# Optimization experiments

Hardware: AMD Instinct MI355X
Metric: run time of the kernel (lower is better)

The kernel has to match this reference:

```python
import jax, jax.numpy as jnp
import numpy as np

B, T, V = 32, 100, 20000
E, H, M, DD = 128, 128, 64, 2


def setup_inputs() -> dict:
    key = jax.random.key(0)
    ks = jax.random.split(key, 12)
    x = jax.random.uniform(ks[0], (B, T, V), dtype=jnp.float32)
    # zero out trailing timesteps per example so Masking layer matters
    lens = jax.random.randint(ks[1], (B,), T * 3 // 4, T + 1)
    tmask = (jnp.arange(T)[None, :] < lens[:, None]).astype(jnp.float32)
    x = x * tmask[:, :, None]
    a = jax.random.uniform(ks[2], (B, V), dtype=jnp.float32)
    d = jax.random.normal(ks[3], (B, DD), dtype=jnp.float32)
    # parameters
    emb = jax.random.uniform(ks[4], (V, E), minval=-0.1, maxval=0.1, dtype=jnp.float32)
    s = 1.0 / np.sqrt(E)
    gru_k = jax.random.uniform(ks[5], (E, 3 * H), minval=-s, maxval=s, dtype=jnp.float32)
    gru_rk = jax.random.normal(ks[6], (H, 3 * H), dtype=jnp.float32) / np.sqrt(H)
    gru_b_i = jnp.zeros((3 * H,), jnp.float32)   # input bias (reset_after=True)
    gru_b_r = jnp.zeros((3 * H,), jnp.float32)   # recurrent bias
    s1 = 1.0 / np.sqrt(H + E)
    W1 = jax.random.uniform(ks[7], (H + E, M), minval=-s1, maxval=s1, dtype=jnp.float32)
    b1 = jnp.zeros((M,), jnp.float32)
    s2 = 1.0 / np.sqrt(M + DD)
    W2 = jax.random.uniform(ks[8], (M + DD, 1), minval=-s2, maxval=s2, dtype=jnp.float32)
    b2 = jnp.zeros((1,), jnp.float32)
    return dict(x=x, a=a, d=d, emb=emb, gru_k=gru_k, gru_rk=gru_rk,
                gru_b_i=gru_b_i, gru_b_r=gru_b_r, W1=W1, b1=b1, W2=W2, b2=b2)


def _gru_final_state(xe, mask, gru_k, gru_rk, gru_b_i, gru_b_r):
    # xe: [B,T,E], mask: [B,T] bool. Keras GRU, reset_after=True, eval mode (dropout off).
    Hn = gru_rk.shape[0]
    x_proj = jnp.einsum('bte,eh->bth', xe, gru_k) + gru_b_i  # [B,T,3H]

    def step(h, inp):
        xp_t, m_t = inp                      # [B,3H], [B]
        rec = h @ gru_rk + gru_b_r           # [B,3H]
        xz, xr, xh = jnp.split(xp_t, 3, axis=-1)
        rz, rr, rh = jnp.split(rec, 3, axis=-1)
        z = jax.nn.sigmoid(xz + rz)
        r = jax.nn.sigmoid(xr + rr)
        hh = jnp.tanh(xh + r * rh)
        h_new = z * h + (1.0 - z) * hh
        h = jnp.where(m_t[:, None], h_new, h)  # masked steps carry state
        return h, None

    h0 = jnp.zeros((xe.shape[0], Hn), xe.dtype)
    h_final, _ = jax.lax.scan(step, h0, (jnp.swapaxes(x_proj, 0, 1), jnp.swapaxes(mask, 0, 1)))
    return h_final


def reference(x, a, d, emb, gru_k, gru_rk, gru_b_i, gru_b_r, W1, b1, W2, b2):
    ae = jnp.tanh(a @ emb)                       # [B,E]
    xe = jnp.tanh(jnp.einsum('btv,ve->bte', x, emb))  # [B,T,E]
    mask = jnp.any(xe != 0.0, axis=-1)           # Masking(mask_value=0.0)
    h = _gru_final_state(xe, mask, gru_k, gru_rk, gru_b_i, gru_b_r)  # [B,H]
    c = jnp.tanh(jnp.concatenate([h, ae], axis=1) @ W1 + b1)         # [B,M]
    out = jax.nn.sigmoid(jnp.concatenate([c, d], axis=1) @ W2 + b2)  # [B,1]
    return out
```

## Files before the change

### kernel.cpp

```cpp
#include <hip/hip_runtime.h>

typedef __attribute__((ext_vector_type(8))) short short8;
typedef __attribute__((ext_vector_type(4))) float float4v;

#define V_ 20000

__device__ __forceinline__ unsigned short f2bf(float f) {
    union { float f; unsigned int u; } v; v.f = f;
    unsigned int u = v.u;
    u += 0x7fffu + ((u >> 16) & 1u);
    return (unsigned short)(u >> 16);
}

__device__ __forceinline__ float fast_tanh(float x) {
    float xc = fminf(15.f, fmaxf(-15.f, x));
    float e = __expf(2.f * xc);
    return (e - 1.f) / (e + 1.f);
}

__device__ __forceinline__ float sigmoidf_(float x) {
    float xc = fminf(30.f, fmaxf(-30.f, x));
    return 1.f / (1.f + __expf(-xc));
}

#define GLL16(gp, lp) __builtin_amdgcn_global_load_lds( \
    (const __attribute__((address_space(1))) void*)(gp), \
    (__attribute__((address_space(3))) void*)(lp), 16, 0, 0)

__global__ __launch_bounds__(256) void cvt_embT(const float* __restrict__ emb,
                                                unsigned short* __restrict__ embT,
                                                float* __restrict__ xeacc) {
    int tid = threadIdx.x;
    int gid = blockIdx.x * 256 + tid;
    for (int i = gid; i < 3328 * 128; i += 313 * 256) xeacc[i] = 0.f;

    __shared__ unsigned short tile[128 * 65];
    int k0 = blockIdx.x * 64;
    const float4v* e4 = (const float4v*)emb;
    #pragma unroll
    for (int c = 0; c < 8; ++c) {
        int l4 = c * 256 + tid;
        int k = l4 >> 5;
        int n4 = l4 & 31;
        float4v f = {0.f, 0.f, 0.f, 0.f};
        if (k0 + k < V_) f = e4[(size_t)(k0 + k) * 32 + n4];
        tile[(n4 * 4 + 0) * 65 + k] = f2bf(f.x);
        tile[(n4 * 4 + 1) * 65 + k] = f2bf(f.y);
        tile[(n4 * 4 + 2) * 65 + k] = f2bf(f.z);
        tile[(n4 * 4 + 3) * 65 + k] = f2bf(f.w);
    }
    __syncthreads();
    #pragma unroll
    for (int c = 0; c < 4; ++c) {
        int l8 = c * 256 + tid;
        int n = l8 >> 3, seg = l8 & 7;
        int kk = k0 + seg * 8;
        if (kk < V_) {
            short8 v;
            #pragma unroll
            for (int i = 0; i < 8; ++i) v[i] = (short)tile[n * 65 + seg * 8 + i];
            *(short8*)(embT + (size_t)n * V_ + kk) = v;
        }
    }
}

__global__ __launch_bounds__(256, 4) void big_gemm(const float* __restrict__ x,
                                                   const float* __restrict__ a,
                                                   const unsigned short* __restrict__ embT,
                                                   float* __restrict__ xeacc,
                                                   int ks) {
    __shared__ unsigned short Alds[2][128 * 40];
    __shared__ unsigned short Blds[2][128 * 32];
    int tid = threadIdx.x;
    int bx = blockIdx.x, by = blockIdx.y;
    int m0 = bx * 128;
    int per = 625 / ks, extra = 625 % ks;
    int kb0 = by * per + (by < extra ? by : extra);
    int nkb = per + (by < extra ? 1 : 0);

    int lane = tid & 63, wave = tid >> 6;
    int wr = wave >> 1, wc = wave & 1;
    int ln = lane & 15, quad = lane >> 4;

    float4v acc[4][4];
    #pragma unroll
    for (int i = 0; i < 4; ++i)
        #pragma unroll
        for (int j = 0; j < 4; ++j) acc[i][j] = (float4v){0.f, 0.f, 0.f, 0.f};

    int row = tid >> 1, seg = tid & 1;
    int rg = m0 + row;
    int aidx = rg - 3200; aidx = aidx < 0 ? 0 : (aidx > 31 ? 31 : aidx);
    const float* __restrict__ srcA = (rg < 3200) ? (x + (size_t)rg * V_)
                                                 : (a + (size_t)aidx * V_);
    int brow0 = tid >> 2, bkq = tid & 3;
    int wbase = tid & ~63;
    const unsigned short* gB0 = embT + (size_t)brow0 * V_ + bkq * 8;
    const unsigned short* gB1 = embT + (size_t)(64 + brow0) * V_ + bkq * 8;

    float4v fa0, fa1, fa2, fa3;

    {
        int k0 = kb0 * 32;
        const float4v* ap = (const float4v*)(srcA + k0 + seg * 16);
        fa0 = ap[0]; fa1 = ap[1]; fa2 = ap[2]; fa3 = ap[3];
        GLL16(gB0 + k0, &Blds[0][(size_t)wbase * 8]);
        GLL16(gB1 + k0, &Blds[0][(size_t)(256 + wbase) * 8]);
        short8 w0, w1;
        w0[0]=(short)f2bf(fa0.x); w0[1]=(short)f2bf(fa0.y); w0[2]=(short)f2bf(fa0.z); w0[3]=(short)f2bf(fa0.w);
        w0[4]=(short)f2bf(fa1.x); w0[5]=(short)f2bf(fa1.y); w0[6]=(short)f2bf(fa1.z); w0[7]=(short)f2bf(fa1.w);
        w1[0]=(short)f2bf(fa2.x); w1[1]=(short)f2bf(fa2.y); w1[2]=(short)f2bf(fa2.z); w1[3]=(short)f2bf(fa2.w);
        w1[4]=(short)f2bf(fa3.x); w1[5]=(short)f2bf(fa3.y); w1[6]=(short)f2bf(fa3.z); w1[7]=(short)f2bf(fa3.w);
        *(short8*)&Alds[0][row * 40 + seg * 16]     = w0;
        *(short8*)&Alds[0][row * 40 + seg * 16 + 8] = w1;
    }
    __syncthreads();

    for (int it = 0; it < nkb; ++it) {
        int buf = it & 1, nxt = buf ^ 1;
        bool more = (it + 1 < nkb);
        if (more) {
            int k0 = (kb0 + it + 1) * 32;
            const float4v* ap = (const float4v*)(srcA + k0 + seg * 16);
            fa0 = ap[0]; fa1 = ap[1]; fa2 = ap[2]; fa3 = ap[3];
            GLL16(gB0 + k0, &Blds[nxt][(size_t)wbase * 8]);
            GLL16(gB1 + k0, &Blds[nxt][(size_t)(256 + wbase) * 8]);
        }
        short8 af[4];
        #pragma unroll
        for (int i = 0; i < 4; ++i)
            af[i] = *(const short8*)&Alds[buf][(wr * 64 + i * 16 + ln) * 40 + quad * 8];
        #pragma unroll
        for (int j = 0; j < 4; ++j) {
            short8 bf = *(const short8*)&Blds[buf][(wc * 64 + j * 16 + ln) * 32 + quad * 8];
            #pragma unroll
            for (int i = 0; i < 4; ++i)
                acc[i][j] = __builtin_amdgcn_mfma_f32_16x16x32_bf16(af[i], bf, acc[i][j], 0, 0, 0);
        }
        if (more) {
            short8 w0, w1;
            w0[0]=(short)f2bf(fa0.x); w0[1]=(short)f2bf(fa0.y); w0[2]=(short)f2bf(fa0.z); w0[3]=(short)f2bf(fa0.w);
            w0[4]=(short)f2bf(fa1.x); w0[5]=(short)f2bf(fa1.y); w0[6]=(short)f2bf(fa1.z); w0[7]=(short)f2bf(fa1.w);
            w1[0]=(short)f2bf(fa2.x); w1[1]=(short)f2bf(fa2.y); w1[2]=(short)f2bf(fa2.z); w1[3]=(short)f2bf(fa2.w);
            w1[4]=(short)f2bf(fa3.x); w1[5]=(short)f2bf(fa3.y); w1[6]=(short)f2bf(fa3.z); w1[7]=(short)f2bf(fa3.w);
            *(short8*)&Alds[nxt][row * 40 + seg * 16]     = w0;
            *(short8*)&Alds[nxt][row * 40 + seg * 16 + 8] = w1;
        }
        __syncthreads();
    }

    #pragma unroll
    for (int i = 0; i < 4; ++i) {
        #pragma unroll
        for (int j = 0; j < 4; ++j) {
            int rowb = m0 + wr * 64 + i * 16 + quad * 4;
            int col = wc * 64 + j * 16 + ln;
            #pragma unroll
            for (int r = 0; r < 4; ++r)
                unsafeAtomicAdd(&xeacc[(size_t)(rowb + r) * 128 + col], acc[i][j][r]);
        }
    }
}

__global__ __launch_bounds__(384) void xproj_fused(const float* __restrict__ xeacc,
                                                   const float* __restrict__ gru_k,
                                                   const float* __restrict__ b_i,
                                                   float* __restrict__ xproj,
                                                   float* __restrict__ maskg,
                                                   float* __restrict__ ae) {
    int tid = threadIdx.x;
    if (blockIdx.x == 200) {
        for (int i = tid; i < 32 * 128; i += 384)
            ae[i] = fast_tanh(xeacc[3200 * 128 + i]);
        return;
    }
    __shared__ float xs[16 * 128];
    __shared__ int anyr[16];
    int row0 = blockIdx.x * 16;
    if (tid < 16) anyr[tid] = 0;
    __syncthreads();
    for (int i = tid; i < 2048; i += 384) {
        float v = fast_tanh(xeacc[(size_t)row0 * 128 + i]);
        xs[i] = v;
        if (v != 0.f) anyr[i >> 7] = 1;
    }
    __syncthreads();
    if (tid < 16) maskg[row0 + tid] = anyr[tid] ? 1.f : 0.f;

    int j = tid;
    float acc[16];
    #pragma unroll
    for (int r = 0; r < 16; ++r) acc[r] = 0.f;
    float bi = b_i[j];
    for (int k4 = 0; k4 < 32; ++k4) {
        float g0 = gru_k[(k4 * 4 + 0) * 384 + j];
        float g1 = gru_k[(k4 * 4 + 1) * 384 + j];
        float g2 = gru_k[(k4 * 4 + 2) * 384 + j];
        float g3 = gru_k[(k4 * 4 + 3) * 384 + j];
        #pragma unroll
        for (int r = 0; r < 16; ++r) {
            float4v xv = *(const float4v*)&xs[r * 128 + k4 * 4];
            acc[r] = fmaf(xv.x, g0, acc[r]);
            acc[r] = fmaf(xv.y, g1, acc[r]);
            acc[r] = fmaf(xv.z, g2, acc[r]);
            acc[r] = fmaf(xv.w, g3, acc[r]);
        }
    }
    #pragma unroll
    for (int r = 0; r < 16; ++r)
        xproj[(size_t)(row0 + r) * 384 + j] = acc[r] + bi;
}

__global__ __launch_bounds__(384) void gru_fused(const float* __restrict__ xproj,
                                                 const float* __restrict__ maskg,
                                                 const float* __restrict__ gru_rk,
                                                 const float* __restrict__ b_r,
                                                 const float* __restrict__ ae,
                                                 const float* __restrict__ d,
                                                 const float* __restrict__ W1,
                                                 const float* __restrict__ b1,
                                                 const float* __restrict__ W2,
                                                 const float* __restrict__ b2,
                                                 float* __restrict__ out) {
    int b = blockIdx.x;
    int j = threadIdx.x;
    float w[128];
    #pragma unroll
    for (int k = 0; k < 128; ++k) w[k] = gru_rk[k * 384 + j];
    float br = b_r[j];
    __shared__ float4v hs4[32];
    __shared__ float recs[384];
    float* hs = (float*)hs4;
    float hreg = 0.f;
    if (j < 128) hs[j] = 0.f;
    const float* xp_base = xproj + (size_t)b * 100 * 384;
    const float* mk = maskg + b * 100;
    float xz = 0.f, xr = 0.f, xh = 0.f;
    if (j < 128) { xz = xp_base[j]; xr = xp_base[128 + j]; xh = xp_base[256 + j]; }
    __syncthreads();
    for (int t = 0; t < 100; ++t) {
        float nxz = 0.f, nxr = 0.f, nxh = 0.f;
        if (t < 99 && j < 128) {
            const float* nb = xp_base + (t + 1) * 384;
            nxz = nb[j]; nxr = nb[128 + j]; nxh = nb[256 + j];
        }
        float s0 = 0.f, s1 = 0.f, s2 = 0.f, s3 = 0.f;
        #pragma unroll
        for (int k4 = 0; k4 < 32; ++k4) {
            float4v hv = hs4[k4];
            s0 = fmaf(hv.x, w[k4 * 4 + 0], s0);
            s1 = fmaf(hv.y, w[k4 * 4 + 1], s1);
            s2 = fmaf(hv.z, w[k4 * 4 + 2], s2);
            s3 = fmaf(hv.w, w[k4 * 4 + 3], s3);
        }
        recs[j] = br + ((s0 + s1) + (s2 + s3));
        __syncthreads();
        if (j < 128) {
            float z = sigmoidf_(xz + recs[j]);
            float r = sigmoidf_(xr + recs[128 + j]);
            float hh = fast_tanh(xh + r * recs[256 + j]);
            float hn = z * hreg + (1.f - z) * hh;
            hreg = (mk[t] != 0.f) ? hn : hreg;
            hs[j] = hreg;
        }
        __syncthreads();
        xz = nxz; xr = nxr; xh = nxh;
    }
    if (j < 64) {
        int m = j;
        float s = b1[m];
        const float* ab = ae + b * 128;
        #pragma unroll 4
        for (int k = 0; k < 128; ++k) s = fmaf(hs[k], W1[k * 64 + m], s);
        #pragma unroll 4
        for (int k = 0; k < 128; ++k) s = fmaf(ab[k], W1[(128 + k) * 64 + m], s);
        float c = fast_tanh(s);
        float p = c * W2[m];
        #pragma unroll
        for (int off = 32; off > 0; off >>= 1) p += __shfl_down(p, off);
        if (m == 0) {
            p += d[b * 2 + 0] * W2[64] + d[b * 2 + 1] * W2[65] + b2[0];
            out[b] = sigmoidf_(p);
        }
    }
}

extern "C" void kernel_launch(void* const* d_in, const int* in_sizes, int n_in,
                              void* d_out, int out_size, void* d_ws, size_t ws_size,
                              hipStream_t stream) {
    (void)in_sizes; (void)n_in; (void)out_size; (void)ws_size;
    const float* x      = (const float*)d_in[0];
    const float* a      = (const float*)d_in[1];
    const float* d      = (const float*)d_in[2];
    const float* emb    = (const float*)d_in[3];
    const float* gru_k  = (const float*)d_in[4];
    const float* gru_rk = (const float*)d_in[5];
    const float* gbi    = (const float*)d_in[6];
    const float* gbr    = (const float*)d_in[7];
    const float* W1     = (const float*)d_in[8];
    const float* b1     = (const float*)d_in[9];
    const float* W2     = (const float*)d_in[10];
    const float* b2     = (const float*)d_in[11];
    float* out = (float*)d_out;

    char* ws = (char*)d_ws;
    unsigned short* embT = (unsigned short*)(ws);
    float* xeacc   = (float*)(ws + 5120000);
    float* ae      = (float*)(ws + 6823936);
    float* maskg   = (float*)(ws + 6840320);
    float* xproj   = (float*)(ws + 6853120);

    const int ks = 32;

    hipLaunchKernelGGL(cvt_embT,    dim3(313),    dim3(256), 0, stream, emb, embT, xeacc);
    hipLaunchKernelGGL(big_gemm,    dim3(26, ks), dim3(256), 0, stream, x, a, embT, xeacc, ks);
    hipLaunchKernelGGL(xproj_fused, dim3(201),    dim3(384), 0, stream, xeacc, gru_k, gbi, xproj, maskg, ae);
    hipLaunchKernelGGL(gru_fused,   dim3(32),     dim3(384), 0, stream, xproj, maskg, gru_rk, gbr,
                       ae, d, W1, b1, W2, b2, out);
}
```

Measured before the change: 573.4 us.

## Replace atomic split-K accumulation with per-slice partial buffers reduced downstream

The big GEMM now writes each K-split's tile to its own partial slice with plain stores instead of atomically adding into a shared zero-initialized accumulator. The xproj kernel sums the slices with vectorized loads before applying tanh and the mask test. This drops the zeroing pass and the atomic contention. The split-K factor falls from 32 to 16 and is halved further if the workspace is too small. In exchange, the partial buffers cost more memory traffic, and the reduction loop adds work to the xproj kernel.

After: 564.9 us. Within noise of the previous version (-1.5%).

```diff
diff --git a/kernel.cpp b/kernel.cpp
--- a/kernel.cpp
+++ b/kernel.cpp
@@ -28,13 +28,9 @@
     (__attribute__((address_space(3))) void*)(lp), 16, 0, 0)
 
 __global__ __launch_bounds__(256) void cvt_embT(const float* __restrict__ emb,
-                                                unsigned short* __restrict__ embT,
-                                                float* __restrict__ xeacc) {
+                                                unsigned short* __restrict__ embT) {
+    __shared__ unsigned short tile[128 * 65];
     int tid = threadIdx.x;
-    int gid = blockIdx.x * 256 + tid;
-    for (int i = gid; i < 3328 * 128; i += 313 * 256) xeacc[i] = 0.f;
-
-    __shared__ unsigned short tile[128 * 65];
     int k0 = blockIdx.x * 64;
     const float4v* e4 = (const float4v*)emb;
     #pragma unroll
@@ -67,7 +63,7 @@
 __global__ __launch_bounds__(256, 4) void big_gemm(const float* __restrict__ x,
                                                    const float* __restrict__ a,
                                                    const unsigned short* __restrict__ embT,
-                                                   float* __restrict__ xeacc,
+                                                   float* __restrict__ partial,
                                                    int ks) {
     __shared__ unsigned short Alds[2][128 * 40];
     __shared__ unsigned short Blds[2][128 * 32];
@@ -149,6 +145,7 @@
         __syncthreads();
     }
 
+    float* dst = partial + (size_t)by * 3328 * 128;
     #pragma unroll
     for (int i = 0; i < 4; ++i) {
         #pragma unroll
@@ -157,21 +154,26 @@
             int col = wc * 64 + j * 16 + ln;
             #pragma unroll
             for (int r = 0; r < 4; ++r)
-                unsafeAtomicAdd(&xeacc[(size_t)(rowb + r) * 128 + col], acc[i][j][r]);
-        }
-    }
-}
-
-__global__ __launch_bounds__(384) void xproj_fused(const float* __restrict__ xeacc,
+                dst[(size_t)(rowb + r) * 128 + col] = acc[i][j][r];
+        }
+    }
+}
+
+__global__ __launch_bounds__(384) void xproj_fused(const float* __restrict__ partial,
                                                    const float* __restrict__ gru_k,
                                                    const float* __restrict__ b_i,
                                                    float* __restrict__ xproj,
                                                    float* __restrict__ maskg,
-                                                   float* __restrict__ ae) {
+                                                   float* __restrict__ ae,
+                                                   int ks) {
+    const size_t SL = (size_t)3328 * 128;
     int tid = threadIdx.x;
     if (blockIdx.x == 200) {
-        for (int i = tid; i < 32 * 128; i += 384)
-            ae[i] = fast_tanh(xeacc[3200 * 128 + i]);
+        for (int i = tid; i < 32 * 128; i += 384) {
+            float s = 0.f;
+            for (int k = 0; k < ks; ++k) s += partial[(size_t)k * SL + 3200 * 128 + i];
+            ae[i] = fast_tanh(s);
+        }
         return;
     }
     __shared__ float xs[16 * 128];
@@ -179,10 +181,20 @@
     int row0 = blockIdx.x * 16;
     if (tid < 16) anyr[tid] = 0;
     __syncthreads();
-    for (int i = tid; i < 2048; i += 384) {
-        float v = fast_tanh(xeacc[(size_t)row0 * 128 + i]);
-        xs[i] = v;
-        if (v != 0.f) anyr[i >> 7] = 1;
+    const float4v* p4 = (const float4v*)partial + (size_t)row0 * 32;
+    const size_t SL4 = SL / 4;
+    for (int i4 = tid; i4 < 512; i4 += 384) {
+        float4v s = p4[i4];
+        for (int k = 1; k < ks; ++k) {
+            float4v t = p4[(size_t)k * SL4 + i4];
+            s.x += t.x; s.y += t.y; s.z += t.z; s.w += t.w;
+        }
+        float4v v;
+        v.x = fast_tanh(s.x); v.y = fast_tanh(s.y);
+        v.z = fast_tanh(s.z); v.w = fast_tanh(s.w);
+        *(float4v*)&xs[i4 * 4] = v;
+        if (v.x != 0.f || v.y != 0.f || v.z != 0.f || v.w != 0.f)
+            anyr[i4 >> 5] = 1;
     }
     __syncthreads();
     if (tid < 16) maskg[row0 + tid] = anyr[tid] ? 1.f : 0.f;
@@ -288,7 +300,7 @@
 extern "C" void kernel_launch(void* const* d_in, const int* in_sizes, int n_in,
                               void* d_out, int out_size, void* d_ws, size_t ws_size,
                               hipStream_t stream) {
-    (void)in_sizes; (void)n_in; (void)out_size; (void)ws_size;
+    (void)in_sizes; (void)n_in; (void)out_size;
     const float* x      = (const float*)d_in[0];
     const float* a      = (const float*)d_in[1];
     const float* d      = (const float*)d_in[2];
@@ -305,16 +317,22 @@
 
     char* ws = (char*)d_ws;
     unsigned short* embT = (unsigned short*)(ws);
-    float* xeacc   = (float*)(ws + 5120000);
-    float* ae      = (float*)(ws + 6823936);
-    float* maskg   = (float*)(ws + 6840320);
-    float* xproj   = (float*)(ws + 6853120);
-
-    const int ks = 32;
-
-    hipLaunchKernelGGL(cvt_embT,    dim3(313),    dim3(256), 0, stream, emb, embT, xeacc);
-    hipLaunchKernelGGL(big_gemm,    dim3(26, ks), dim3(256), 0, stream, x, a, embT, xeacc, ks);
-    hipLaunchKernelGGL(xproj_fused, dim3(201),    dim3(384), 0, stream, xeacc, gru_k, gbi, xproj, maskg, ae);
+    const size_t slice = (size_t)3328 * 128 * 4;
+    float* partial = (float*)(ws + 5120000);
+
+    int ks = 16;
+    {
+        size_t fixed_rest = 16384 + 12800 + 4915200;
+        while (ks > 1 && 5120000 + (size_t)ks * slice + fixed_rest > ws_size) ks >>= 1;
+    }
+    char* after = ws + 5120000 + (size_t)ks * slice;
+    float* ae      = (float*)(after);
+    float* maskg   = (float*)(after + 16384);
+    float* xproj   = (float*)(after + 29184);
+
+    hipLaunchKernelGGL(cvt_embT,    dim3(313),    dim3(256), 0, stream, emb, embT);
+    hipLaunchKernelGGL(big_gemm,    dim3(26, ks), dim3(256), 0, stream, x, a, embT, partial, ks);
+    hipLaunchKernelGGL(xproj_fused, dim3(201),    dim3(384), 0, stream, partial, gru_k, gbi, xproj, maskg, ae, ks);
     hipLaunchKernelGGL(gru_fused,   dim3(32),     dim3(384), 0, stream, xproj, maskg, gru_rk, gbr,
                        ae, d, W1, b1, W2, b2, out);
 }
```
